# Kernel optimization log

Measured on AMD Instinct MI355X. Metric: run time of the kernel, lower is better.

Reference implementation:

```python
import jax, jax.numpy as jnp
import numpy as np

TEMPERATURE = 0.1  # init kwarg
EPS = 1e-8        # torch cosine_similarity eps


def setup_inputs() -> dict:
    key = jax.random.key(0)
    k1, k2, k3 = jax.random.split(key, 3)
    B, D, C = 4096, 1024, 32
    representations = jax.random.normal(k1, (B, D), dtype=jnp.float32)
    soft_labels = jax.random.uniform(k2, (B, C), dtype=jnp.float32)
    labels = jax.random.randint(k3, (B,), 0, 32, dtype=jnp.int64)
    return {
        "representations": representations,
        "soft_labels": soft_labels,
        "labels": labels,
        "pseudo_weight": 10,
    }


def reference(representations, soft_labels, labels, pseudo_weight):
    B = representations.shape[0]
    # row-normalize (cosine similarity)
    norms = jnp.maximum(jnp.linalg.norm(representations, axis=1, keepdims=True), EPS)
    rn = representations / norms
    Z = (rn @ rn.T) / TEMPERATURE                      # [B, B] scaled cosine sims
    E = jnp.exp(Z)
    off_diag = 1.0 - jnp.eye(B, dtype=Z.dtype)         # exclude j == i
    denom = jnp.sum(E * off_diag, axis=1, keepdims=True)   # [B, 1]
    loss_arr = -(Z - jnp.log(denom))                   # -log(exp(Z_ij)/denom_i)
    # positive-pair weights: same label, j != i (detached in original)
    pos = (labels[:, None] == labels[None, :]).astype(Z.dtype) * off_diag
    soft_sim = jax.lax.stop_gradient(soft_labels @ soft_labels.T)  # torch.inner, detached
    w = pos + pseudo_weight * soft_sim
    return jnp.sum(loss_arr * w) / B
```

## Files before the change

### kernel.cpp

```cpp
#include <hip/hip_runtime.h>
#include <hip/hip_bf16.h>
#include <stdint.h>


typedef float f32x4 __attribute__((ext_vector_type(4)));
typedef long i64;

#define INV_T 10.0f
#define Z_SCALE (INV_T / 256.0f)

#define CHUNK_STRIDE 262144

#define OFF_RNF8  0
#define OFF_DENOM 4194304
#define OFF_POSS  (OFF_DENOM + 16384)
#define OFF_G     (OFF_POSS + 16384)
#define OFF_OACC  (OFF_G + 131072)
#define OFF_DONE  (OFF_OACC + 16)
#define ZERO_SPAN 167936
#define OFF_CSP   (OFF_DENOM + ZERO_SPAN)
#define OFF_CCP   (OFF_CSP + 4096)
#define OFF_W     (OFF_CCP + 4096)

#define N_GEMM 528
#define N_G    512
#define N_W    16

__global__ __launch_bounds__(256) void scl_stage1(const float* __restrict__ rep,
                                                  const float* __restrict__ sl,
                                                  const int* __restrict__ labels,
                                                  uint8_t* __restrict__ rnf8,
                                                  float* __restrict__ cs_part,
                                                  int* __restrict__ cc_part,
                                                  char* __restrict__ zbase) {
    int b = blockIdx.x;
    int t = threadIdx.x;
    if (b < 4096) {
        int row = b;
        const float4* src = reinterpret_cast<const float4*>(rep + (size_t)row * 1024);
        float4 v = src[t];
        float s = v.x * v.x + v.y * v.y + v.z * v.z + v.w * v.w;
#pragma unroll
        for (int m = 1; m < 64; m <<= 1) s += __shfl_xor(s, m, 64);
        __shared__ float red[4];
        if ((t & 63) == 0) red[t >> 6] = s;
        __syncthreads();
        s = red[0] + red[1] + red[2] + red[3];
        float nf = 16.0f / fmaxf(sqrtf(s), 1e-8f);
        int p = 0;
        p = __builtin_amdgcn_cvt_pk_fp8_f32(v.x * nf, v.y * nf, p, false);
        p = __builtin_amdgcn_cvt_pk_fp8_f32(v.z * nf, v.w * nf, p, true);
        *(uint32_t*)&rnf8[(size_t)(t >> 4) * CHUNK_STRIDE + row * 64 + (t & 15) * 4] =
            (uint32_t)p;
    } else if (b < 4128) {
        __shared__ float part[8][32];
        __shared__ int bins[32];
        int bb = b - 4096;
        if (t < 32) bins[t] = 0;
        __syncthreads();
        if (t < 128) atomicAdd(&bins[labels[bb * 128 + t]], 1);
        int c = t & 31, rg = t >> 5;
        float s = 0.f;
#pragma unroll 4
        for (int k = 0; k < 16; ++k) {
            int i = bb * 128 + rg * 16 + k;
            s += sl[i * 32 + c];
        }
        part[rg][c] = s;
        __syncthreads();
        if (t < 32) {
            float tot = 0.f;
#pragma unroll
            for (int g = 0; g < 8; ++g) tot += part[g][t];
            cs_part[bb * 32 + t] = tot;
            cc_part[bb * 32 + t] = bins[t];
        }
    } else {
        int zb = b - 4128;
        *(uint4*)(zbase + (size_t)zb * 4096 + t * 16) = (uint4){0, 0, 0, 0};
    }
}

__global__ __launch_bounds__(256) void scl_gw(const uint8_t* __restrict__ rnf8,
                                              const float* __restrict__ sl,
                                              const int* __restrict__ labels,
                                              const float* __restrict__ cs_part,
                                              const int* __restrict__ cc_part,
                                              const int* __restrict__ pwp,
                                              float* __restrict__ G,
                                              float* __restrict__ W) {
    int tid = threadIdx.x;
    int bIdx = blockIdx.x;

    if (bIdx < N_G) {
        __shared__ __align__(16) uint8_t rns[128 * 64];
        __shared__ __align__(16) float sls[128 * 32];
        int dblk = bIdx & 15, ks = bIdx >> 4;
        int i0 = ks * 128;
        const uint8_t* slab = rnf8 + (size_t)dblk * CHUNK_STRIDE + (size_t)i0 * 64;
#pragma unroll
        for (int p = 0; p < 2; ++p) {
            int off = p * 4096 + tid * 16;
            *(uint4*)&rns[off] = *(const uint4*)&slab[off];
        }
#pragma unroll
        for (int p = 0; p < 4; ++p) {
            int off = p * 1024 + tid * 4;
            *(float4*)&sls[off] = *(const float4*)&sl[(size_t)i0 * 32 + off];
        }
        __syncthreads();
        int dq = tid >> 5, c = tid & 31;
        int d0 = dblk * 64 + dq * 8;
        float acc[8];
#pragma unroll
        for (int j = 0; j < 8; ++j) acc[j] = 0.f;
#pragma unroll 4
        for (int k = 0; k < 128; ++k) {
            uint2 rv = *(const uint2*)&rns[k * 64 + dq * 8];
            float sv = sls[k * 32 + c];
            acc[0] += __builtin_amdgcn_cvt_f32_fp8((int)rv.x, 0) * sv;
            acc[1] += __builtin_amdgcn_cvt_f32_fp8((int)rv.x, 1) * sv;
            acc[2] += __builtin_amdgcn_cvt_f32_fp8((int)rv.x, 2) * sv;
            acc[3] += __builtin_amdgcn_cvt_f32_fp8((int)rv.x, 3) * sv;
            acc[4] += __builtin_amdgcn_cvt_f32_fp8((int)rv.y, 0) * sv;
            acc[5] += __builtin_amdgcn_cvt_f32_fp8((int)rv.y, 1) * sv;
            acc[6] += __builtin_amdgcn_cvt_f32_fp8((int)rv.y, 2) * sv;
            acc[7] += __builtin_amdgcn_cvt_f32_fp8((int)rv.y, 3) * sv;
        }
#pragma unroll
        for (int j = 0; j < 8; ++j)
            atomicAdd(&G[(d0 + j) * 32 + c], acc[j] * 0.0625f);
    } else {
        __shared__ __align__(16) float css[32];
        __shared__ int ccs[32];
        if (tid < 32) {
            float s = 0.f; int n = 0;
#pragma unroll
            for (int b = 0; b < 32; ++b) { s += cs_part[b * 32 + tid]; n += cc_part[b * 32 + tid]; }
            css[tid] = s; ccs[tid] = n;
        }
        __syncthreads();
        int bits = *pwp;
        float pw = (bits >= -(1 << 22) && bits <= (1 << 22)) ? (float)bits
                                                             : __int_as_float(bits);
        int i = (bIdx - N_G) * 256 + tid;
        const f32x4* sl4 = (const f32x4*)sl;
        const f32x4* cs4 = (const f32x4*)css;
        float dW = 0.f;
#pragma unroll
        for (int q = 0; q < 8; ++q) {
            f32x4 s = sl4[i * 8 + q];
            f32x4 c = cs4[q];
            dW += s[0] * c[0] + s[1] * c[1] + s[2] * c[2] + s[3] * c[3];
        }
        W[i] = (float)(ccs[labels[i]] - 1) + pw * dW;
    }
}

__global__ __launch_bounds__(256) void scl_gemm(const uint8_t* __restrict__ rnf8,
                                                const int* __restrict__ labels,
                                                float* __restrict__ denom,
                                                float* __restrict__ posS) {
    int tid = threadIdx.x;
    int bIdx = blockIdx.x;

    __shared__ int lblA[128], lblB[128];

    int L = (bIdx & 7) * 66 + (bIdx >> 3);
    int bi = 0, rem = L;
    while (rem >= 32 - bi) { rem -= 32 - bi; ++bi; }
    int bj = bi + rem;
    int rowA0 = bi * 128, colB0 = bj * 128;

    if (tid < 128) {
        lblA[tid] = labels[rowA0 + tid];
        lblB[tid] = labels[colB0 + tid];
    }
    __syncthreads();

    int lane = tid & 63, warp = tid >> 6;
    int wr = warp >> 1, wc = warp & 1;
    int m_ = lane & 15, g = lane >> 4;

    const uint8_t* gAf = rnf8 + (size_t)(rowA0 + wr * 64 + m_) * 64 + g * 16;
    const uint8_t* gBf = rnf8 + (size_t)(colB0 + wc * 64 + m_) * 64 + g * 16;

    f32x4 acc[4][4];
#pragma unroll
    for (int a = 0; a < 4; ++a)
#pragma unroll
        for (int b = 0; b < 4; ++b) acc[a][b] = (f32x4){0.f, 0.f, 0.f, 0.f};

    f32x4 a0[4], b0[4], a1[4], b1[4];

#define MFMA_SET(AF, BF)                                                       \
    _Pragma("unroll") for (int s = 0; s < 2; ++s)                              \
        _Pragma("unroll") for (int ti = 0; ti < 4; ++ti)                       \
            _Pragma("unroll") for (int tj = 0; tj < 4; ++tj) {                 \
                i64 av = ((const i64*)&AF[ti])[s];                             \
                i64 bv = ((const i64*)&BF[tj])[s];                             \
                acc[ti][tj] = __builtin_amdgcn_mfma_f32_16x16x32_fp8_fp8(      \
                    av, bv, acc[ti][tj], 0, 0, 0);                             \
            }

#pragma unroll
    for (int t = 0; t < 4; ++t) {
        a0[t] = *(const f32x4*)(gAf + t * 1024);
        b0[t] = *(const f32x4*)(gBf + t * 1024);
    }
    for (int kt = 0; kt < 16; kt += 2) {
        size_t c1 = (size_t)(kt + 1) * CHUNK_STRIDE;
#pragma unroll
        for (int t = 0; t < 4; ++t) {
            a1[t] = *(const f32x4*)(gAf + c1 + t * 1024);
            b1[t] = *(const f32x4*)(gBf + c1 + t * 1024);
        }
        MFMA_SET(a0, b0);
        if (kt + 2 < 16) {
            size_t c2 = (size_t)(kt + 2) * CHUNK_STRIDE;
#pragma unroll
            for (int t = 0; t < 4; ++t) {
                a0[t] = *(const f32x4*)(gAf + c2 + t * 1024);
                b0[t] = *(const f32x4*)(gBf + c2 + t * 1024);
            }
        }
        MFMA_SET(a1, b1);
    }
#undef MFMA_SET

    bool isDiag = (bi == bj);
    int cl = m_;
    float colE[4] = {0.f, 0.f, 0.f, 0.f}, colP[4] = {0.f, 0.f, 0.f, 0.f};
#pragma unroll
    for (int ti = 0; ti < 4; ++ti) {
        int rowLoc = wr * 64 + ti * 16 + g * 4;
        float rE[4] = {0.f, 0.f, 0.f, 0.f}, rP[4] = {0.f, 0.f, 0.f, 0.f};
        int lr[4];
#pragma unroll
        for (int r = 0; r < 4; ++r) lr[r] = lblA[rowLoc + r];
#pragma unroll
        for (int tj = 0; tj < 4; ++tj) {
            int colLoc = wc * 64 + tj * 16 + cl;
            int gCol = colB0 + colLoc;
            int lc = lblB[colLoc];
            f32x4 a = acc[ti][tj];
#pragma unroll
            for (int r = 0; r < 4; ++r) {
                int gRow = rowA0 + rowLoc + r;
                float z = Z_SCALE * a[r];
                float e = __expf(z);
                bool offd = (gRow != gCol);
                if (!offd) e = 0.f;
                rE[r] += e;
                colE[tj] += e;
                if (offd && (lr[r] == lc)) { rP[r] += z; colP[tj] += z; }
            }
        }
#pragma unroll
        for (int r = 0; r < 4; ++r) {
            float v = rE[r], p = rP[r];
#pragma unroll
            for (int msk = 1; msk < 16; msk <<= 1) {
                v += __shfl_xor(v, msk, 64);
                p += __shfl_xor(p, msk, 64);
            }
            if (cl == 0) {
                int gRow = rowA0 + rowLoc + r;
                atomicAdd(&denom[gRow], v);
                atomicAdd(&posS[gRow], p);
            }
        }
    }
    if (!isDiag) {
#pragma unroll
        for (int tj = 0; tj < 4; ++tj) {
            float v = colE[tj], p = colP[tj];
            v += __shfl_xor(v, 16, 64); p += __shfl_xor(p, 16, 64);
            v += __shfl_xor(v, 32, 64); p += __shfl_xor(p, 32, 64);
            if (g == 0) {
                int gCol = colB0 + wc * 64 + tj * 16 + cl;
                atomicAdd(&denom[gCol], v);
                atomicAdd(&posS[gCol], p);
            }
        }
    }
}

__global__ __launch_bounds__(256) void scl_finalize(const float* __restrict__ denom,
                                                    const float* __restrict__ posS,
                                                    const float* __restrict__ W,
                                                    const float* __restrict__ G,
                                                    const int* __restrict__ pwp,
                                                    double* __restrict__ oacc,
                                                    int* __restrict__ done,
                                                    float* __restrict__ out) {
    int t = threadIdx.x;
    __shared__ double wsum[4];
    double contrib = 0.0;

    if (blockIdx.x < 8) {
        int i0 = blockIdx.x * 512 + t;
        float t0 = __logf(denom[i0]) * W[i0] - posS[i0];
        float t1 = __logf(denom[i0 + 256]) * W[i0 + 256] - posS[i0 + 256];
        double td = (double)t0 + (double)t1;
#pragma unroll
        for (int m = 1; m < 64; m <<= 1) td += __shfl_xor(td, m, 64);
        if ((t & 63) == 0) wsum[t >> 6] = td;
        __syncthreads();
        contrib = wsum[0] + wsum[1] + wsum[2] + wsum[3];
    } else {
        int bits = *pwp;
        float pw = (bits >= -(1 << 22) && bits <= (1 << 22)) ? (float)bits
                                                             : __int_as_float(bits);
        const f32x4* G4 = (const f32x4*)G;
        float gs = 0.f;
#pragma unroll
        for (int q = 0; q < 32; ++q) {
            f32x4 v = G4[q * 256 + t];
            gs += v[0] * v[0] + v[1] * v[1] + v[2] * v[2] + v[3] * v[3];
        }
        double gd = (double)gs;
#pragma unroll
        for (int m = 1; m < 64; m <<= 1) gd += __shfl_xor(gd, m, 64);
        if ((t & 63) == 0) wsum[t >> 6] = gd;
        __syncthreads();
        contrib = -(double)(pw * INV_T) * (wsum[0] + wsum[1] + wsum[2] + wsum[3]);
    }

    if (t == 0) {
        atomicAdd(oacc, contrib);
        __threadfence();
        int old = atomicAdd(done, 1);
        if (old == 8) {
            double tot = atomicAdd(oacc, 0.0);
            out[0] = (float)(tot * (1.0 / 4096.0));
        }
    }
}

extern "C" void kernel_launch(void* const* d_in, const int* in_sizes, int n_in,
                              void* d_out, int out_size, void* d_ws, size_t ws_size,
                              hipStream_t stream) {
    const float* rep = (const float*)d_in[0];
    const float* sl = (const float*)d_in[1];
    const int* labels = (const int*)d_in[2];
    const int* pwp = (const int*)d_in[3];

    char* ws = (char*)d_ws;
    uint8_t* rnf8 = (uint8_t*)(ws + OFF_RNF8);
    float* denom = (float*)(ws + OFF_DENOM);
    float* posS = (float*)(ws + OFF_POSS);
    float* G = (float*)(ws + OFF_G);
    double* oacc = (double*)(ws + OFF_OACC);
    int* done = (int*)(ws + OFF_DONE);
    float* cs_part = (float*)(ws + OFF_CSP);
    int* cc_part = (int*)(ws + OFF_CCP);
    float* W = (float*)(ws + OFF_W);

    scl_stage1<<<4169, 256, 0, stream>>>(rep, sl, labels, rnf8,
                                         cs_part, cc_part, ws + OFF_DENOM);
    scl_gw<<<N_G + N_W, 256, 0, stream>>>(rnf8, sl, labels, cs_part, cc_part,
                                          pwp, G, W);
    scl_gemm<<<N_GEMM, 256, 0, stream>>>(rnf8, labels, denom, posS);
    scl_finalize<<<9, 256, 0, stream>>>(denom, posS, W, G, pwp, oacc, done,
                                        (float*)d_out);
}
```

Before: 124.0 us.

## Merge GW and GEMM kernels into one launch and triple-buffer fp8 loads

Combines the G/W side-computation kernel and the fp8 MFMA gram kernel into one launch. GEMM tiles take the low block indices and the G/W blocks run after them, which removes a launch boundary and lets the two kinds of work share the GPU at the same time. The GEMM K-loop changes from double-buffered to fully unrolled triple-buffered register prefetch, so global loads are issued two chunks ahead of the MFMAs. This raises register pressure, which may lower occupancy, and the merged kernel's register and shared-memory footprint now applies to the light G/W blocks too.

```diff
diff --git a/kernel.cpp b/kernel.cpp
--- a/kernel.cpp
+++ b/kernel.cpp
@@ -25,6 +25,7 @@
 #define N_GEMM 528
 #define N_G    512
 #define N_W    16
+#define N_ALL  (N_GEMM + N_G + N_W)
 
 __global__ __launch_bounds__(256) void scl_stage1(const float* __restrict__ rep,
                                                   const float* __restrict__ sl,
@@ -81,88 +82,86 @@
     }
 }
 
-__global__ __launch_bounds__(256) void scl_gw(const uint8_t* __restrict__ rnf8,
-                                              const float* __restrict__ sl,
-                                              const int* __restrict__ labels,
-                                              const float* __restrict__ cs_part,
-                                              const int* __restrict__ cc_part,
-                                              const int* __restrict__ pwp,
-                                              float* __restrict__ G,
-                                              float* __restrict__ W) {
+__global__ __launch_bounds__(256) void scl_main(const uint8_t* __restrict__ rnf8,
+                                                const float* __restrict__ sl,
+                                                const int* __restrict__ labels,
+                                                const float* __restrict__ cs_part,
+                                                const int* __restrict__ cc_part,
+                                                const int* __restrict__ pwp,
+                                                float* __restrict__ denom,
+                                                float* __restrict__ posS,
+                                                float* __restrict__ G,
+                                                float* __restrict__ W) {
     int tid = threadIdx.x;
     int bIdx = blockIdx.x;
 
-    if (bIdx < N_G) {
-        __shared__ __align__(16) uint8_t rns[128 * 64];
-        __shared__ __align__(16) float sls[128 * 32];
-        int dblk = bIdx & 15, ks = bIdx >> 4;
-        int i0 = ks * 128;
-        const uint8_t* slab = rnf8 + (size_t)dblk * CHUNK_STRIDE + (size_t)i0 * 64;
-#pragma unroll
-        for (int p = 0; p < 2; ++p) {
-            int off = p * 4096 + tid * 16;
-            *(uint4*)&rns[off] = *(const uint4*)&slab[off];
-        }
-#pragma unroll
-        for (int p = 0; p < 4; ++p) {
-            int off = p * 1024 + tid * 4;
-            *(float4*)&sls[off] = *(const float4*)&sl[(size_t)i0 * 32 + off];
-        }
-        __syncthreads();
-        int dq = tid >> 5, c = tid & 31;
-        int d0 = dblk * 64 + dq * 8;
-        float acc[8];
-#pragma unroll
-        for (int j = 0; j < 8; ++j) acc[j] = 0.f;
+    if (bIdx >= N_GEMM) {
+        if (bIdx < N_GEMM + N_G) {
+            __shared__ __align__(16) uint8_t rns[128 * 64];
+            __shared__ __align__(16) float sls[128 * 32];
+            int idx = bIdx - N_GEMM;
+            int dblk = idx & 15, ks = idx >> 4;
+            int i0 = ks * 128;
+            const uint8_t* slab = rnf8 + (size_t)dblk * CHUNK_STRIDE + (size_t)i0 * 64;
+#pragma unroll
+            for (int p = 0; p < 2; ++p) {
+                int off = p * 4096 + tid * 16;
+                *(uint4*)&rns[off] = *(const uint4*)&slab[off];
+            }
+#pragma unroll
+            for (int p = 0; p < 4; ++p) {
+                int off = p * 1024 + tid * 4;
+                *(float4*)&sls[off] = *(const float4*)&sl[(size_t)i0 * 32 + off];
+            }
+            __syncthreads();
+            int dq = tid >> 5, c = tid & 31;
+            int d0 = dblk * 64 + dq * 8;
+            float acc[8];
+#pragma unroll
+            for (int j = 0; j < 8; ++j) acc[j] = 0.f;
 #pragma unroll 4
-        for (int k = 0; k < 128; ++k) {
-            uint2 rv = *(const uint2*)&rns[k * 64 + dq * 8];
-            float sv = sls[k * 32 + c];
-            acc[0] += __builtin_amdgcn_cvt_f32_fp8((int)rv.x, 0) * sv;
-            acc[1] += __builtin_amdgcn_cvt_f32_fp8((int)rv.x, 1) * sv;
-            acc[2] += __builtin_amdgcn_cvt_f32_fp8((int)rv.x, 2) * sv;
-            acc[3] += __builtin_amdgcn_cvt_f32_fp8((int)rv.x, 3) * sv;
-            acc[4] += __builtin_amdgcn_cvt_f32_fp8((int)rv.y, 0) * sv;
-            acc[5] += __builtin_amdgcn_cvt_f32_fp8((int)rv.y, 1) * sv;
-            acc[6] += __builtin_amdgcn_cvt_f32_fp8((int)rv.y, 2) * sv;
-            acc[7] += __builtin_amdgcn_cvt_f32_fp8((int)rv.y, 3) * sv;
-        }
-#pragma unroll
-        for (int j = 0; j < 8; ++j)
-            atomicAdd(&G[(d0 + j) * 32 + c], acc[j] * 0.0625f);
-    } else {
-        __shared__ __align__(16) float css[32];
-        __shared__ int ccs[32];
-        if (tid < 32) {
-            float s = 0.f; int n = 0;
-#pragma unroll
-            for (int b = 0; b < 32; ++b) { s += cs_part[b * 32 + tid]; n += cc_part[b * 32 + tid]; }
-            css[tid] = s; ccs[tid] = n;
-        }
-        __syncthreads();
-        int bits = *pwp;
-        float pw = (bits >= -(1 << 22) && bits <= (1 << 22)) ? (float)bits
-                                                             : __int_as_float(bits);
-        int i = (bIdx - N_G) * 256 + tid;
-        const f32x4* sl4 = (const f32x4*)sl;
-        const f32x4* cs4 = (const f32x4*)css;
-        float dW = 0.f;
-#pragma unroll
-        for (int q = 0; q < 8; ++q) {
-            f32x4 s = sl4[i * 8 + q];
-            f32x4 c = cs4[q];
-            dW += s[0] * c[0] + s[1] * c[1] + s[2] * c[2] + s[3] * c[3];
-        }
-        W[i] = (float)(ccs[labels[i]] - 1) + pw * dW;
-    }
-}
-
-__global__ __launch_bounds__(256) void scl_gemm(const uint8_t* __restrict__ rnf8,
-                                                const int* __restrict__ labels,
-                                                float* __restrict__ denom,
-                                                float* __restrict__ posS) {
-    int tid = threadIdx.x;
-    int bIdx = blockIdx.x;
+            for (int k = 0; k < 128; ++k) {
+                uint2 rv = *(const uint2*)&rns[k * 64 + dq * 8];
+                float sv = sls[k * 32 + c];
+                acc[0] += __builtin_amdgcn_cvt_f32_fp8((int)rv.x, 0) * sv;
+                acc[1] += __builtin_amdgcn_cvt_f32_fp8((int)rv.x, 1) * sv;
+                acc[2] += __builtin_amdgcn_cvt_f32_fp8((int)rv.x, 2) * sv;
+                acc[3] += __builtin_amdgcn_cvt_f32_fp8((int)rv.x, 3) * sv;
+                acc[4] += __builtin_amdgcn_cvt_f32_fp8((int)rv.y, 0) * sv;
+                acc[5] += __builtin_amdgcn_cvt_f32_fp8((int)rv.y, 1) * sv;
+                acc[6] += __builtin_amdgcn_cvt_f32_fp8((int)rv.y, 2) * sv;
+                acc[7] += __builtin_amdgcn_cvt_f32_fp8((int)rv.y, 3) * sv;
+            }
+#pragma unroll
+            for (int j = 0; j < 8; ++j)
+                atomicAdd(&G[(d0 + j) * 32 + c], acc[j] * 0.0625f);
+        } else {
+            __shared__ __align__(16) float css[32];
+            __shared__ int ccs[32];
+            if (tid < 32) {
+                float s = 0.f; int n = 0;
+#pragma unroll
+                for (int b = 0; b < 32; ++b) { s += cs_part[b * 32 + tid]; n += cc_part[b * 32 + tid]; }
+                css[tid] = s; ccs[tid] = n;
+            }
+            __syncthreads();
+            int bits = *pwp;
+            float pw = (bits >= -(1 << 22) && bits <= (1 << 22)) ? (float)bits
+                                                                 : __int_as_float(bits);
+            int i = (bIdx - (N_GEMM + N_G)) * 256 + tid;
+            const f32x4* sl4 = (const f32x4*)sl;
+            const f32x4* cs4 = (const f32x4*)css;
+            float dW = 0.f;
+#pragma unroll
+            for (int q = 0; q < 8; ++q) {
+                f32x4 s = sl4[i * 8 + q];
+                f32x4 c = cs4[q];
+                dW += s[0] * c[0] + s[1] * c[1] + s[2] * c[2] + s[3] * c[3];
+            }
+            W[i] = (float)(ccs[labels[i]] - 1) + pw * dW;
+        }
+        return;
+    }
 
     __shared__ int lblA[128], lblB[128];
 
@@ -191,7 +190,7 @@
 #pragma unroll
         for (int b = 0; b < 4; ++b) acc[a][b] = (f32x4){0.f, 0.f, 0.f, 0.f};
 
-    f32x4 a0[4], b0[4], a1[4], b1[4];
+    f32x4 a0[4], b0[4], a1[4], b1[4], a2[4], b2[4];
 
 #define MFMA_SET(AF, BF)                                                       \
     _Pragma("unroll") for (int s = 0; s < 2; ++s)                              \
@@ -202,30 +201,35 @@
                 acc[ti][tj] = __builtin_amdgcn_mfma_f32_16x16x32_fp8_fp8(      \
                     av, bv, acc[ti][tj], 0, 0, 0);                             \
             }
-
-#pragma unroll
-    for (int t = 0; t < 4; ++t) {
-        a0[t] = *(const f32x4*)(gAf + t * 1024);
-        b0[t] = *(const f32x4*)(gBf + t * 1024);
-    }
-    for (int kt = 0; kt < 16; kt += 2) {
-        size_t c1 = (size_t)(kt + 1) * CHUNK_STRIDE;
-#pragma unroll
-        for (int t = 0; t < 4; ++t) {
-            a1[t] = *(const f32x4*)(gAf + c1 + t * 1024);
-            b1[t] = *(const f32x4*)(gBf + c1 + t * 1024);
-        }
-        MFMA_SET(a0, b0);
-        if (kt + 2 < 16) {
-            size_t c2 = (size_t)(kt + 2) * CHUNK_STRIDE;
-#pragma unroll
-            for (int t = 0; t < 4; ++t) {
-                a0[t] = *(const f32x4*)(gAf + c2 + t * 1024);
-                b0[t] = *(const f32x4*)(gBf + c2 + t * 1024);
-            }
-        }
-        MFMA_SET(a1, b1);
-    }
+#define LOADF(AF, BF, KT)                                                      \
+    {                                                                          \
+        size_t co = (size_t)(KT) * CHUNK_STRIDE;                               \
+        _Pragma("unroll") for (int t = 0; t < 4; ++t) {                        \
+            AF[t] = *(const f32x4*)(gAf + co + t * 1024);                      \
+            BF[t] = *(const f32x4*)(gBf + co + t * 1024);                      \
+        }                                                                      \
+    }
+
+    LOADF(a0, b0, 0)
+    LOADF(a1, b1, 1)
+    LOADF(a2, b2, 2)
+    MFMA_SET(a0, b0) LOADF(a0, b0, 3)
+    MFMA_SET(a1, b1) LOADF(a1, b1, 4)
+    MFMA_SET(a2, b2) LOADF(a2, b2, 5)
+    MFMA_SET(a0, b0) LOADF(a0, b0, 6)
+    MFMA_SET(a1, b1) LOADF(a1, b1, 7)
+    MFMA_SET(a2, b2) LOADF(a2, b2, 8)
+    MFMA_SET(a0, b0) LOADF(a0, b0, 9)
+    MFMA_SET(a1, b1) LOADF(a1, b1, 10)
+    MFMA_SET(a2, b2) LOADF(a2, b2, 11)
+    MFMA_SET(a0, b0) LOADF(a0, b0, 12)
+    MFMA_SET(a1, b1) LOADF(a1, b1, 13)
+    MFMA_SET(a2, b2) LOADF(a2, b2, 14)
+    MFMA_SET(a0, b0) LOADF(a0, b0, 15)
+    MFMA_SET(a1, b1)
+    MFMA_SET(a2, b2)
+    MFMA_SET(a0, b0)
+#undef LOADF
 #undef MFMA_SET
 
     bool isDiag = (bi == bj);
@@ -359,9 +363,8 @@
 
     scl_stage1<<<4169, 256, 0, stream>>>(rep, sl, labels, rnf8,
                                          cs_part, cc_part, ws + OFF_DENOM);
-    scl_gw<<<N_G + N_W, 256, 0, stream>>>(rnf8, sl, labels, cs_part, cc_part,
-                                          pwp, G, W);
-    scl_gemm<<<N_GEMM, 256, 0, stream>>>(rnf8, labels, denom, posS);
+    scl_main<<<N_ALL, 256, 0, stream>>>(rnf8, sl, labels, cs_part, cc_part, pwp,
+                                        denom, posS, G, W);
     scl_finalize<<<9, 256, 0, stream>>>(denom, posS, W, G, pwp, oacc, done,
                                         (float*)d_out);
 }
```

Measured after the change: 116.1 us, median of 2. 6.4% less time.
